# Kernel optimization log

Hardware: AMD Instinct MI355X
Metric: run time of the kernel (lower is better)

## Reference

```python
import jax, jax.numpy as jnp
import numpy as np

B, NSIDE, NH = 4, 64, 8
N = 12 * NSIDE * NSIDE          # HEALPix pixel count, nested ordering
CIN, CHID, COUT = 256, 512, 256
WS = 16                          # window = 4**(w+1) nested pixels, w=1
HD = CHID // NH


def _ln(x, g, b, eps=1e-5):
    m = x.mean(-1, keepdims=True)
    v = ((x - m) ** 2).mean(-1, keepdims=True)
    return (x - m) * jax.lax.rsqrt(v + eps) * g + b


def _win_attn(x, qkv_w, qkv_b, pw, pb):
    b_, n_, c = x.shape
    nw = n_ // WS
    xw = x.reshape(b_, nw, WS, c)
    qkv = xw @ qkv_w + qkv_b                      # [B, nw, ws, 3C]
    q, k, v = jnp.split(qkv, 3, axis=-1)
    def heads(t):
        return t.reshape(b_, nw, WS, NH, HD).transpose(0, 1, 3, 2, 4)
    q, k, v = heads(q), heads(k), heads(v)        # [B, nw, H, ws, hd]
    a = jax.nn.softmax(jnp.einsum('bwhqd,bwhkd->bwhqk', q, k) * (HD ** -0.5), axis=-1)
    o = jnp.einsum('bwhqk,bwhkd->bwhqd', a, v)
    o = o.transpose(0, 1, 3, 2, 4).reshape(b_, n_, c)
    return o @ pw + pb


def _heal_block(x, p, shift):
    if shift:
        x = jnp.roll(x, -WS // 2, axis=1)          # shifted-window (cyclic in nested order)
    x = x + _win_attn(_ln(x, p['ln1g'], p['ln1b']), p['qkvw'], p['qkvb'], p['pw'], p['pb'])
    h = _ln(x, p['ln2g'], p['ln2b'])
    h = jax.nn.gelu(h @ p['m1w'] + p['m1b'], approximate=False) @ p['m2w'] + p['m2b']
    x = x + h
    if shift:
        x = jnp.roll(x, WS // 2, axis=1)
    return x


def _sn_linear(h, W, b, u):
    # torch spectral_norm: one power-iteration, u/v detached, sigma = u' W v
    v = W @ u                                      # [CHID]
    v = jax.lax.stop_gradient(v / (jnp.linalg.norm(v) + 1e-12))
    u2 = v @ W                                     # [COUT]
    u2 = jax.lax.stop_gradient(u2 / (jnp.linalg.norm(u2) + 1e-12))
    sigma = v @ W @ u2
    return h @ (W / sigma) + b


def setup_inputs() -> dict:
    key = jax.random.key(0)
    ks = iter(jax.random.split(key, 64))
    def w(shape, s=0.02):
        return jax.random.normal(next(ks), shape, jnp.float32) * s
    inp = {'x': jax.random.normal(next(ks), (B, N, CIN), jnp.float32)}
    inp['ff1_w'] = w((CIN, CHID)); inp['ff1_b'] = jnp.zeros((CHID,), jnp.float32)
    for pre in ('a', 'b'):
        inp[f'{pre}_ln1g'] = jnp.ones((CHID,), jnp.float32)
        inp[f'{pre}_ln1b'] = jnp.zeros((CHID,), jnp.float32)
        inp[f'{pre}_qkvw'] = w((CHID, 3 * CHID)); inp[f'{pre}_qkvb'] = jnp.zeros((3 * CHID,), jnp.float32)
        inp[f'{pre}_pw'] = w((CHID, CHID)); inp[f'{pre}_pb'] = jnp.zeros((CHID,), jnp.float32)
        inp[f'{pre}_ln2g'] = jnp.ones((CHID,), jnp.float32)
        inp[f'{pre}_ln2b'] = jnp.zeros((CHID,), jnp.float32)
        inp[f'{pre}_m1w'] = w((CHID, 4 * CHID)); inp[f'{pre}_m1b'] = jnp.zeros((4 * CHID,), jnp.float32)
        inp[f'{pre}_m2w'] = w((4 * CHID, CHID)); inp[f'{pre}_m2b'] = jnp.zeros((CHID,), jnp.float32)
    inp['ff2_w'] = w((CHID, COUT)); inp['ff2_b'] = jnp.zeros((COUT,), jnp.float32)
    inp['ff2_u'] = jax.random.normal(next(ks), (COUT,), jnp.float32)
    return inp


def reference(x, ff1_w, ff1_b,
              a_ln1g, a_ln1b, a_qkvw, a_qkvb, a_pw, a_pb, a_ln2g, a_ln2b, a_m1w, a_m1b, a_m2w, a_m2b,
              b_ln1g, b_ln1b, b_qkvw, b_qkvb, b_pw, b_pb, b_ln2g, b_ln2b, b_m1w, b_m1b, b_m2w, b_m2b,
              ff2_w, ff2_b, ff2_u):
    pa = dict(ln1g=a_ln1g, ln1b=a_ln1b, qkvw=a_qkvw, qkvb=a_qkvb, pw=a_pw, pb=a_pb,
              ln2g=a_ln2g, ln2b=a_ln2b, m1w=a_m1w, m1b=a_m1b, m2w=a_m2w, m2b=a_m2b)
    pb_ = dict(ln1g=b_ln1g, ln1b=b_ln1b, qkvw=b_qkvw, qkvb=b_qkvb, pw=b_pw, pb=b_pb,
               ln2g=b_ln2g, ln2b=b_ln2b, m1w=b_m1w, m1b=b_m1b, m2w=b_m2w, m2b=b_m2b)
    h = jax.nn.gelu(x @ ff1_w + ff1_b, approximate=False)   # feed_forward1
    h = _heal_block(h, pa, shift=False)                     # message_passing1
    h = _heal_block(h, pb_, shift=True)                     # message_passing2
    return _sn_linear(h, ff2_w, ff2_b, ff2_u)               # spectral-norm linear
```

## Files before the change

kernel.cpp:

```cpp
#include <hip/hip_runtime.h>
#include <hip/hip_bf16.h>
#include <math.h>

typedef _Float16 f16;
typedef __attribute__((ext_vector_type(8))) _Float16 f16x8;
typedef __attribute__((ext_vector_type(4))) _Float16 f16x4;
typedef __attribute__((ext_vector_type(4))) float f32x4;

#define DINLINE __device__ __forceinline__

DINLINE float gelu_fast(float x) {
  float x2 = x * x;
  float z = x * __builtin_fmaf(-0.10294537f, x2, -2.30211422f);
  float E = __builtin_amdgcn_exp2f(z);
  return x * __builtin_amdgcn_rcpf(1.0f + E);
}
DINLINE void gload16(const void* g, void* l) {
  __builtin_amdgcn_global_load_lds((const __attribute__((address_space(1))) void*)g,
                                   (__attribute__((address_space(3))) void*)l, 16, 0, 0);
}

#define BAR       __builtin_amdgcn_s_barrier()
#define WAITLGKM  asm volatile("s_waitcnt lgkmcnt(0)" ::: "memory")
#define WAITVM(n) asm volatile("s_waitcnt vmcnt(" #n ")" ::: "memory")

template <int EPI>
__global__ __launch_bounds__(512, 4) void gemm(
    const f16* __restrict__ A, const f16* __restrict__ Bt,
    const float* __restrict__ bias, const f16* __restrict__ Cin,
    float* __restrict__ Cf, f16* __restrict__ Cb,
    const float* __restrict__ scale_ptr,
    int N, int K, int nct)
{
  __shared__ alignas(16) f16 sm[2][3][4096];

  const int nwg = (int)gridDim.x;
  const int gid = (int)blockIdx.x;
  const int q = nwg >> 3, r = nwg & 7;
  const int xcd = gid & 7, idx = gid >> 3;
  const int swz = (xcd < r ? xcd * (q + 1) : r * (q + 1) + (xcd - r) * q) + idx;
  const int rt = swz / nct, ct = swz - rt * nct;
  const int m0 = rt << 7, n0 = ct << 8;

  const int tid = (int)threadIdx.x;
  const int lane = tid & 63;
  const int wid = tid >> 6;
  const int wr = wid >> 2, wcn = wid & 3;

  const int rsel = lane & 15, khi = lane >> 4;
  const int sx = (khi ^ ((rsel >> 1) & 3)) << 3;

  const int breg = 1 + (wcn >> 1);
  const int brow0 = (wcn & 1) * 64;

  f32x4 acc[4][4] = {};
  f16x8 aF[4], bF[4];

  const int NT = K >> 5;

#define STAGE(b, k0)                                                          \
  {                                                                           \
    _Pragma("unroll")                                                         \
    for (int _g = 0; _g < 3; ++_g) {                                          \
      const int _s = _g * 512 + tid;                                          \
      const int _reg = _s >> 9, _smi = _s & 511;                              \
      const int _row = _smi >> 2;                                             \
      const int _ls = (_smi & 3) ^ ((_row >> 1) & 3);                         \
      const f16* _src = (_reg == 0)                                           \
          ? A + (size_t)(m0 + _row) * K                                       \
          : Bt + (size_t)(n0 + ((_reg - 1) << 7) + _row) * K;                 \
      gload16(_src + (k0) + (_ls << 3), &sm[b][_reg][_smi * 8]);              \
    }                                                                         \
  }

#define DSRA(b)                                                               \
  {                                                                           \
    _Pragma("unroll")                                                         \
    for (int _i = 0; _i < 4; ++_i)                                            \
      aF[_i] = *(const f16x8*)(&sm[b][0][(wr * 64 + _i * 16 + rsel) * 32 + sx]); \
  }

#define DSRB(b)                                                               \
  {                                                                           \
    _Pragma("unroll")                                                         \
    for (int _i = 0; _i < 4; ++_i)                                            \
      bF[_i] = *(const f16x8*)(&sm[b][breg][(brow0 + _i * 16 + rsel) * 32 + sx]); \
  }

#define MMC                                                                   \
  {                                                                           \
    __builtin_amdgcn_s_setprio(1);                                            \
    _Pragma("unroll")                                                         \
    for (int _m = 0; _m < 4; ++_m)                                            \
      _Pragma("unroll")                                                       \
      for (int _n = 0; _n < 4; ++_n)                                          \
        acc[_m][_n] = __builtin_amdgcn_mfma_f32_16x16x32_f16(                 \
            bF[_n], aF[_m], acc[_m][_n], 0, 0, 0);                            \
    __builtin_amdgcn_s_setprio(0);                                            \
  }

  STAGE(0, 0);
  for (int t = 0; t < NT; ++t) {
    const int b = t & 1;
    if (t + 1 < NT) {
      if (b) STAGE(0, (t + 1) << 5) else STAGE(1, (t + 1) << 5)
      WAITVM(3);
    } else {
      WAITVM(0);
    }
    BAR;
    DSRA(b); DSRB(b); WAITLGKM; MMC;
    BAR;
  }

  const float scale = (EPI & 8) ? scale_ptr[0] : 1.0f;
  const int R0 = m0 + wr * 64, C0 = n0 + wcn * 64;
#pragma unroll
  for (int m = 0; m < 4; ++m) {
    const int row = R0 + m * 16 + rsel;
#pragma unroll
    for (int n = 0; n < 4; ++n) {
      const int col = C0 + n * 16 + (khi << 2);
      f32x4 v = acc[m][n];
      if (EPI & 8) {
#pragma unroll
        for (int j = 0; j < 4; ++j) v[j] *= scale;
      }
      f32x4 bb = *(const f32x4*)(bias + col);
#pragma unroll
      for (int j = 0; j < 4; ++j) v[j] += bb[j];
      if (EPI & 1) {
#pragma unroll
        for (int j = 0; j < 4; ++j) v[j] = gelu_fast(v[j]);
      }
      if (EPI & 2) {
        f16x4 c4 = *(const f16x4*)(Cin + (size_t)row * N + col);
#pragma unroll
        for (int j = 0; j < 4; ++j) v[j] += (float)c4[j];
      }
      if (EPI & 4) {
        f16x4 o;
#pragma unroll
        for (int j = 0; j < 4; ++j) o[j] = (f16)v[j];
        *(f16x4*)(Cb + (size_t)row * N + col) = o;
      } else {
        *(f32x4*)(Cf + (size_t)row * N + col) = v;
      }
    }
  }
#undef STAGE
#undef DSRA
#undef DSRB
#undef MMC
}

__global__ __launch_bounds__(256) void ln_f16(
    const f16* __restrict__ X, const float* __restrict__ g,
    const float* __restrict__ b, f16* __restrict__ Y, int ntok)
{
  const int lane = threadIdx.x & 63;
  const int c = lane * 8;
  const f32x4 g0 = *(const f32x4*)(g + c), g1 = *(const f32x4*)(g + c + 4);
  const f32x4 b0 = *(const f32x4*)(b + c), b1 = *(const f32x4*)(b + c + 4);
  for (int token = blockIdx.x * 4 + (threadIdx.x >> 6); token < ntok;
       token += gridDim.x * 4) {
    f16x8 v = *(const f16x8*)(X + (size_t)token * 512 + c);
    float vf[8];
    float s = 0.f, s2 = 0.f;
#pragma unroll
    for (int j = 0; j < 8; ++j) { vf[j] = (float)v[j]; s += vf[j]; s2 += vf[j] * vf[j]; }
#pragma unroll
    for (int o = 32; o > 0; o >>= 1) { s += __shfl_xor(s, o, 64); s2 += __shfl_xor(s2, o, 64); }
    const float mean = s * (1.f / 512.f);
    const float inv = rsqrtf(s2 * (1.f / 512.f) - mean * mean + 1e-5f);
    f16x8 o8;
#pragma unroll
    for (int j = 0; j < 4; ++j) {
      o8[j]     = (f16)((vf[j] - mean) * inv * g0[j] + b0[j]);
      o8[4 + j] = (f16)((vf[4 + j] - mean) * inv * g1[j] + b1[j]);
    }
    *(f16x8*)(Y + (size_t)token * 512 + c) = o8;
  }
}

__global__ __launch_bounds__(256) void cvt_f32_f16(const float* __restrict__ X,
                                                   f16* __restrict__ Y, long n8)
{
  const long i = (long)blockIdx.x * 256 + threadIdx.x;
  if (i >= n8) return;
  f32x4 v0 = *(const f32x4*)(X + i * 8), v1 = *(const f32x4*)(X + i * 8 + 4);
  f16x8 o8;
#pragma unroll
  for (int j = 0; j < 4; ++j) { o8[j] = (f16)v0[j]; o8[4 + j] = (f16)v1[j]; }
  *(f16x8*)(Y + i * 8) = o8;
}

__global__ __launch_bounds__(256) void w_tr_tiled(const float* __restrict__ W,
                                                  f16* __restrict__ Wt, int K, int N)
{
  __shared__ f16 td[64][66];
  const int nkt = K >> 6;
  const int kt = blockIdx.x % nkt, nt = blockIdx.x / nkt;
  const int k0 = kt << 6, n0 = nt << 6;
  const int col = threadIdx.x & 63, rq = threadIdx.x >> 6;
#pragma unroll
  for (int j = 0; j < 16; ++j) {
    const int row = j * 4 + rq;
    td[row][col] = (f16)W[(size_t)(k0 + row) * N + n0 + col];
  }
  __syncthreads();
#pragma unroll
  for (int j = 0; j < 16; ++j) {
    const int nrow = j * 4 + rq;
    Wt[(size_t)(n0 + nrow) * K + k0 + col] = td[col][nrow];
  }
}

template <int SHIFT>
__global__ __launch_bounds__(256) void win_attn(const f16* __restrict__ QKV,
                                                f16* __restrict__ O)
{
  __shared__ alignas(16) f16 kv[2][16][1160];
  const int wl0 = (int)blockIdx.x * 2;
  const int tid = (int)threadIdx.x;

  for (int i = tid; i < 4096; i += 256) {
    const int win = i >> 11;
    const int rem = i & 2047;
    const int row = rem >> 7;
    const int c8 = rem & 127;
    const int src = ((wl0 + win) * 16 + row + SHIFT) % 49152;
    const int sect = c8 >> 6;
    const int hh = (c8 >> 3) & 7;
    const int dd = (c8 & 7) * 8;
    *(f16x8*)(&kv[win][row][sect * 576 + hh * 72 + dd]) =
        *(const f16x8*)(QKV + (size_t)src * 1536 + 512 + c8 * 8);
  }

  const int win = tid >> 7, h = (tid >> 4) & 7, qi = tid & 15;
  const int qtok = ((wl0 + win) * 16 + qi + SHIFT) % 49152;
  f16x8 qv[8];
#pragma unroll
  for (int c8 = 0; c8 < 8; ++c8)
    qv[c8] = *(const f16x8*)(QKV + (size_t)qtok * 1536 + h * 64 + c8 * 8);

  __syncthreads();

  float sc[16];
  float mx = -1e30f;
#pragma unroll
  for (int kj = 0; kj < 16; ++kj) {
    const f16* kr = &kv[win][kj][h * 72];
    float s = 0.f;
#pragma unroll
    for (int c8 = 0; c8 < 8; ++c8) {
      f16x8 k8 = *(const f16x8*)(kr + c8 * 8);
#pragma unroll
      for (int j = 0; j < 8; ++j) s += (float)qv[c8][j] * (float)k8[j];
    }
    s *= 0.125f;
    sc[kj] = s;
    mx = fmaxf(mx, s);
  }
  float sum = 0.f;
#pragma unroll
  for (int kj = 0; kj < 16; ++kj) { sc[kj] = expf(sc[kj] - mx); sum += sc[kj]; }
  const float inv = 1.f / sum;
  float ov[64] = {};
#pragma unroll
  for (int kj = 0; kj < 16; ++kj) {
    const float a = sc[kj] * inv;
    const f16* vr = &kv[win][kj][576 + h * 72];
#pragma unroll
    for (int c8 = 0; c8 < 8; ++c8) {
      f16x8 v8 = *(const f16x8*)(vr + c8 * 8);
#pragma unroll
      for (int j = 0; j < 8; ++j) ov[c8 * 8 + j] += a * (float)v8[j];
    }
  }
  f16* orow = O + (size_t)qtok * 512 + h * 64;
#pragma unroll
  for (int c8 = 0; c8 < 8; ++c8) {
    f16x8 t;
#pragma unroll
    for (int j = 0; j < 8; ++j) t[j] = (f16)ov[c8 * 8 + j];
    *(f16x8*)(orow + c8 * 8) = t;
  }
}

__global__ __launch_bounds__(256) void sn_sigma(const float* __restrict__ W,
                                                const float* __restrict__ u,
                                                float* __restrict__ inv_sigma)
{
  __shared__ float vsh[512];
  __shared__ float ush[256];
  __shared__ float red[256];
  const int t = (int)threadIdx.x;
  ush[t] = u[t];
  __syncthreads();
  float a0 = 0.f, a1 = 0.f;
  for (int j = 0; j < 256; ++j) {
    a0 += W[t * 256 + j] * ush[j];
    a1 += W[(t + 256) * 256 + j] * ush[j];
  }
  vsh[t] = a0; vsh[t + 256] = a1;
  red[t] = a0 * a0 + a1 * a1;
  __syncthreads();
  for (int s = 128; s > 0; s >>= 1) { if (t < s) red[t] += red[t + s]; __syncthreads(); }
  const float nv = sqrtf(red[0]) + 1e-12f;
  __syncthreads();
  const float invv = 1.f / nv;
  vsh[t] *= invv; vsh[t + 256] *= invv;
  __syncthreads();
  float u2 = 0.f;
  for (int i = 0; i < 512; ++i) u2 += vsh[i] * W[i * 256 + t];
  red[t] = u2 * u2;
  __syncthreads();
  for (int s = 128; s > 0; s >>= 1) { if (t < s) red[t] += red[t + s]; __syncthreads(); }
  const float nu = sqrtf(red[0]) + 1e-12f;
  __syncthreads();
  ush[t] = u2 / nu;
  __syncthreads();
  float d0 = 0.f, d1 = 0.f;
  for (int j = 0; j < 256; ++j) {
    d0 += W[t * 256 + j] * ush[j];
    d1 += W[(t + 256) * 256 + j] * ush[j];
  }
  red[t] = vsh[t] * d0 + vsh[t + 256] * d1;
  __syncthreads();
  for (int s = 128; s > 0; s >>= 1) { if (t < s) red[t] += red[t + s]; __syncthreads(); }
  if (t == 0) inv_sigma[0] = 1.f / red[0];
}

__global__ void fill_sentinel(float* __restrict__ out, long n, float val)
{
  const long i = (long)blockIdx.x * 256 + threadIdx.x;
  for (long k = i; k < n; k += (long)gridDim.x * 256) out[k] = val;
}

extern "C" void kernel_launch(void* const* d_in, const int* in_sizes, int n_in,
                              void* d_out, int out_size, void* d_ws, size_t ws_size,
                              hipStream_t stream)
{
  const int M = 196608;
  const int MC = 49152;
  constexpr size_t OFF_U   = 201326592ull;
  constexpr size_t OFF_OH  = 201326592ull + 150994944ull;
  constexpr size_t OFF_WT  = 402653184ull;
  constexpr size_t OFF_SIG = 415760384ull;
  constexpr size_t NEED    = OFF_SIG + 256ull;

  if (ws_size < NEED) {
    fill_sentinel<<<2048, 256, 0, stream>>>((float*)d_out, (long)out_size,
                                            (float)(ws_size >> 20));
    return;
  }

  char* ws = (char*)d_ws;
  f16* R     = (f16*)(ws);
  f16* U     = (f16*)(ws + OFF_U);
  f16* OH    = (f16*)(ws + OFF_OH);
  f16* WT    = (f16*)(ws + OFF_WT);
  float* sig = (float*)(ws + OFF_SIG);
  f16* X     = (f16*)d_out;

  const float* ff1_b = (const float*)d_in[2];
  const float* ff2_b = (const float*)d_in[28];

  f16* W_FF1 = WT;
  auto W_QKV = [&](int blk) { return WT + (blk ? 3276800 : 131072); };
  auto W_PW  = [&](int blk) { return WT + (blk ? 4063232 : 917504); };
  auto W_M1  = [&](int blk) { return WT + (blk ? 4325376 : 1179648); };
  auto W_M2  = [&](int blk) { return WT + (blk ? 5373952 : 2228224); };
  f16* W_FF2 = WT + 6422528;

  w_tr_tiled<<<32, 256, 0, stream>>>((const float*)d_in[1], W_FF1, 256, 512);
  for (int blk = 0; blk < 2; ++blk) {
    w_tr_tiled<<<192, 256, 0, stream>>>((const float*)d_in[blk ? 17 : 5], W_QKV(blk), 512, 1536);
    w_tr_tiled<<<64, 256, 0, stream>>>((const float*)d_in[blk ? 19 : 7], W_PW(blk), 512, 512);
    w_tr_tiled<<<256, 256, 0, stream>>>((const float*)d_in[blk ? 23 : 11], W_M1(blk), 512, 2048);
    w_tr_tiled<<<256, 256, 0, stream>>>((const float*)d_in[blk ? 25 : 13], W_M2(blk), 2048, 512);
  }
  w_tr_tiled<<<32, 256, 0, stream>>>((const float*)d_in[27], W_FF2, 512, 256);
  sn_sigma<<<1, 256, 0, stream>>>((const float*)d_in[27], (const float*)d_in[29], sig);

  cvt_f32_f16<<<24576, 256, 0, stream>>>((const float*)d_in[0], U, (long)M * 256 / 8);
  gemm<5><<<3072, 512, 0, stream>>>(U, W_FF1, ff1_b, nullptr, nullptr, R, nullptr,
                                    512, 256, 2);

  for (int blk = 0; blk < 2; ++blk) {
    const float* ln1g = (const float*)d_in[blk ? 15 : 3];
    const float* ln1b = (const float*)d_in[blk ? 16 : 4];
    const float* qkvb = (const float*)d_in[blk ? 18 : 6];
    const float* pb   = (const float*)d_in[blk ? 20 : 8];
    const float* ln2g = (const float*)d_in[blk ? 21 : 9];
    const float* ln2b = (const float*)d_in[blk ? 22 : 10];
    const float* m1b  = (const float*)d_in[blk ? 24 : 12];
    const float* m2b  = (const float*)d_in[blk ? 26 : 14];

    ln_f16<<<4096, 256, 0, stream>>>(R, ln1g, ln1b, X, M);
    for (int mc = 0; mc < 4; ++mc) {
      const size_t ro = (size_t)mc * MC * 512;
      gemm<4><<<2304, 512, 0, stream>>>(X + ro, W_QKV(blk), qkvb, nullptr,
                                        nullptr, U, nullptr, 1536, 512, 6);
      if (blk == 0) win_attn<0><<<1536, 256, 0, stream>>>(U, OH);
      else          win_attn<8><<<1536, 256, 0, stream>>>(U, OH);
      gemm<6><<<768, 512, 0, stream>>>(OH, W_PW(blk), pb, R + ro,
                                       nullptr, R + ro, nullptr, 512, 512, 2);
    }
    ln_f16<<<4096, 256, 0, stream>>>(R, ln2g, ln2b, X, M);
    for (int mc = 0; mc < 4; ++mc) {
      const size_t ro = (size_t)mc * MC * 512;
      gemm<5><<<3072, 512, 0, stream>>>(X + ro, W_M1(blk), m1b, nullptr,
                                        nullptr, U, nullptr, 2048, 512, 8);
      gemm<6><<<768, 512, 0, stream>>>(U, W_M2(blk), m2b, R + ro,
                                       nullptr, R + ro, nullptr, 512, 2048, 2);
    }
  }

  gemm<8><<<1536, 512, 0, stream>>>(R, W_FF2, ff2_b, nullptr, (float*)d_out,
                                    nullptr, sig, 256, 512, 1);
}
```

Measured before the change: 4.857 ms.

## Restructure GEMM main loop with unrolled double-buffer prefetch and precomputed pointers

Rewrites the GEMM k-loop as a two-step unrolled double-buffered pipeline. The next tile's global-to-LDS loads are issued right after the barrier that follows each compute step, so two tiles are in flight at once. Per-thread global and LDS addresses are precomputed once and advanced by pointer increments, which removes per-iteration index arithmetic and the explicit lgkmcnt wait. The loop assumes an even tile count (K multiple of 64) and relies on compiler-inserted waits for the LDS reads.

Result: no change. 4.794 ms (median of 3 runs) (-1.3%).

```diff
diff --git a/kernel.cpp b/kernel.cpp
--- a/kernel.cpp
+++ b/kernel.cpp
@@ -21,8 +21,8 @@
 }
 
 #define BAR       __builtin_amdgcn_s_barrier()
-#define WAITLGKM  asm volatile("s_waitcnt lgkmcnt(0)" ::: "memory")
 #define WAITVM(n) asm volatile("s_waitcnt vmcnt(" #n ")" ::: "memory")
+#define CFE       asm volatile("" ::: "memory")
 
 template <int EPI>
 __global__ __launch_bounds__(512, 4) void gemm(
@@ -32,7 +32,7 @@
     const float* __restrict__ scale_ptr,
     int N, int K, int nct)
 {
-  __shared__ alignas(16) f16 sm[2][3][4096];
+  __shared__ alignas(16) f16 smf[2 * 3 * 4096];
 
   const int nwg = (int)gridDim.x;
   const int gid = (int)blockIdx.x;
@@ -50,45 +50,36 @@
   const int rsel = lane & 15, khi = lane >> 4;
   const int sx = (khi ^ ((rsel >> 1) & 3)) << 3;
 
-  const int breg = 1 + (wcn >> 1);
-  const int brow0 = (wcn & 1) * 64;
+  const int srow = tid >> 2;
+  const int sls = (tid & 3) ^ ((srow >> 1) & 3);
+  const f16* pA  = A  + (size_t)(m0 + srow) * K + sls * 8;
+  const f16* pB0 = Bt + (size_t)(n0 + srow) * K + sls * 8;
+  const f16* pB1 = Bt + (size_t)(n0 + 128 + srow) * K + sls * 8;
+  f16* ldst = smf + tid * 8;
+
+  const int aB = (wr * 64 + rsel) * 32 + sx;
+  const int bB = (1 + (wcn >> 1)) * 4096 + ((wcn & 1) * 64 + rsel) * 32 + sx;
 
   f32x4 acc[4][4] = {};
-  f16x8 aF[4], bF[4];
-
   const int NT = K >> 5;
 
-#define STAGE(b, k0)                                                          \
+#define STG(boff)                                                             \
   {                                                                           \
-    _Pragma("unroll")                                                         \
-    for (int _g = 0; _g < 3; ++_g) {                                          \
-      const int _s = _g * 512 + tid;                                          \
-      const int _reg = _s >> 9, _smi = _s & 511;                              \
-      const int _row = _smi >> 2;                                             \
-      const int _ls = (_smi & 3) ^ ((_row >> 1) & 3);                         \
-      const f16* _src = (_reg == 0)                                           \
-          ? A + (size_t)(m0 + _row) * K                                       \
-          : Bt + (size_t)(n0 + ((_reg - 1) << 7) + _row) * K;                 \
-      gload16(_src + (k0) + (_ls << 3), &sm[b][_reg][_smi * 8]);              \
-    }                                                                         \
-  }
-
-#define DSRA(b)                                                               \
+    gload16(pA,  ldst + (boff));                                              \
+    gload16(pB0, ldst + (boff) + 4096);                                       \
+    gload16(pB1, ldst + (boff) + 8192);                                       \
+    pA += 32; pB0 += 32; pB1 += 32;                                           \
+  }
+
+#define CMP(boff)                                                             \
   {                                                                           \
+    f16x8 aF[4], bF[4];                                                       \
     _Pragma("unroll")                                                         \
     for (int _i = 0; _i < 4; ++_i)                                            \
-      aF[_i] = *(const f16x8*)(&sm[b][0][(wr * 64 + _i * 16 + rsel) * 32 + sx]); \
-  }
-
-#define DSRB(b)                                                               \
-  {                                                                           \
+      aF[_i] = *(const f16x8*)(smf + (boff) + aB + _i * 512);                 \
     _Pragma("unroll")                                                         \
     for (int _i = 0; _i < 4; ++_i)                                            \
-      bF[_i] = *(const f16x8*)(&sm[b][breg][(brow0 + _i * 16 + rsel) * 32 + sx]); \
-  }
-
-#define MMC                                                                   \
-  {                                                                           \
+      bF[_i] = *(const f16x8*)(smf + (boff) + bB + _i * 512);                 \
     __builtin_amdgcn_s_setprio(1);                                            \
     _Pragma("unroll")                                                         \
     for (int _m = 0; _m < 4; ++_m)                                            \
@@ -99,19 +90,22 @@
     __builtin_amdgcn_s_setprio(0);                                            \
   }
 
-  STAGE(0, 0);
-  for (int t = 0; t < NT; ++t) {
-    const int b = t & 1;
-    if (t + 1 < NT) {
-      if (b) STAGE(0, (t + 1) << 5) else STAGE(1, (t + 1) << 5)
-      WAITVM(3);
-    } else {
-      WAITVM(0);
-    }
-    BAR;
-    DSRA(b); DSRB(b); WAITLGKM; MMC;
-    BAR;
-  }
+  STG(0); STG(12288);
+  for (int t = 0; t + 2 < NT; t += 2) {
+    WAITVM(3); BAR; CFE;
+    CMP(0);
+    BAR; CFE;
+    STG(0);
+    WAITVM(3); BAR; CFE;
+    CMP(12288);
+    BAR; CFE;
+    STG(12288);
+  }
+  WAITVM(3); BAR; CFE;
+  CMP(0);
+  BAR; CFE;
+  WAITVM(0); BAR; CFE;
+  CMP(12288);
 
   const float scale = (EPI & 8) ? scale_ptr[0] : 1.0f;
   const int R0 = m0 + wr * 64, C0 = n0 + wcn * 64;
@@ -148,10 +142,8 @@
       }
     }
   }
-#undef STAGE
-#undef DSRA
-#undef DSRB
-#undef MMC
+#undef STG
+#undef CMP
 }
 
 __global__ __launch_bounds__(256) void ln_f16(
```
